# Optimization experiments

Measured on AMD Instinct MI355X. Metric: run time of the kernel, lower is better.

## Reference

```python
import jax, jax.numpy as jnp
import numpy as np

N = 131072          # total sampled proposals (flattened over batch)
D = 1024            # num_extractor_out
C = 21              # num_classes (VOC: 20 + background)


def setup_inputs() -> dict:
    key = jax.random.key(0)
    k1, k2, k3 = jax.random.split(key, 3)
    features = jax.random.normal(k1, (N, D), dtype=jnp.float32)
    # Linear weights stored as [in, out] so y = x @ W + b
    W_cls = jax.random.normal(k2, (D, C), dtype=jnp.float32) * (1.0 / np.sqrt(D))
    b_cls = jnp.zeros((C,), dtype=jnp.float32)
    W_tf = jax.random.normal(k3, (D, C * 4), dtype=jnp.float32) * (1.0 / np.sqrt(D))
    b_tf = jnp.zeros((C * 4,), dtype=jnp.float32)
    return {"features": features, "W_cls": W_cls, "b_cls": b_cls, "W_tf": W_tf, "b_tf": b_tf}


def reference(features, W_cls, b_cls, W_tf, b_tf):
    # ROI.forward with identity extractor / no pre/post transforms.
    proposal_classes = features @ W_cls + b_cls                    # [N, C]
    proposal_transformers = features @ W_tf + b_tf                 # [N, C*4]
    proposal_transformers = proposal_transformers.reshape(features.shape[0], C, 4)
    return proposal_classes, proposal_transformers
```

## Files before the change

kernel.cpp:

```cpp
#include <hip/hip_runtime.h>
#include <hip/hip_bf16.h>

#define NROWS 131072
#define DK    1024
#define CCLS  21
#define CTF   84
#define NCOL  105
#define NKT   (DK/32)
#define NCT   7
#define BM    128

typedef __attribute__((ext_vector_type(4))) float f32x4;
typedef __attribute__((ext_vector_type(8))) short bf16x8;

__device__ __forceinline__ unsigned short f2bf_rne(float x) {
    union { float f; unsigned u; } v; v.f = x;
    unsigned r = v.u + 0x7fffu + ((v.u >> 16) & 1u);
    return (unsigned short)(r >> 16);
}

__device__ __forceinline__ unsigned pack2(float lo, float hi) {
    union { float f; unsigned u; } a, b; a.f = lo; b.f = hi;
    return ((a.u + 0x8000u) >> 16) | ((b.u + 0x8000u) & 0xffff0000u);
}

__device__ __forceinline__ bf16x8 cvt8(const f32x4 lo, const f32x4 hi) {
    union { unsigned u[4]; bf16x8 v; } r;
    r.u[0] = pack2(lo[0], lo[1]);
    r.u[1] = pack2(lo[2], lo[3]);
    r.u[2] = pack2(hi[0], hi[1]);
    r.u[3] = pack2(hi[2], hi[3]);
    return r.v;
}

__global__ void pack_B_kernel(const float* __restrict__ Wc,
                              const float* __restrict__ Wt,
                              unsigned short* __restrict__ Bp) {
    const int frag = blockIdx.x;
    const int kt = frag / NCT, ct = frag % NCT;
    const int lane = threadIdx.x;
    const int col = ct * 16 + (lane & 15);
    const int k0  = kt * 32 + ((lane >> 4) << 3);
    bf16x8 o;
#pragma unroll
    for (int j = 0; j < 8; ++j) {
        const int k = k0 + j;
        float v = 0.0f;
        if (col < CCLS)      v = Wc[k * CCLS + col];
        else if (col < NCOL) v = Wt[k * CTF + (col - CCLS)];
        o[j] = (short)f2bf_rne(v);
    }
    *reinterpret_cast<bf16x8*>(Bp + ((size_t)frag * 64 + lane) * 8) = o;
}

__global__ __launch_bounds__(256, 4)
void roi_gemm_kernel(const float* __restrict__ F,
                     const unsigned short* __restrict__ Bp,
                     const float* __restrict__ bcls,
                     const float* __restrict__ btf,
                     float* __restrict__ out) {
    const int t    = threadIdx.x;
    const int wave = t >> 6;
    const int lane = t & 63;
    const int fr   = lane & 15;
    const int fk   = (lane >> 4) * 8;

    const long rw = (long)blockIdx.x * BM + wave * 32;
    const float* pa0 = F + (size_t)(rw + fr) * DK + fk;
    const float* pa1 = pa0 + (size_t)16 * DK;

    f32x4 acc[2][NCT];
#pragma unroll
    for (int a = 0; a < 2; ++a)
#pragma unroll
        for (int b = 0; b < NCT; ++b)
            acc[a][b] = (f32x4){0.f, 0.f, 0.f, 0.f};

    const unsigned short* bb = Bp + (size_t)lane * 8;

    for (int kt = 0; kt < NKT; ++kt) {
        const f32x4 a0lo = *reinterpret_cast<const f32x4*>(pa0 + kt * 32);
        const f32x4 a0hi = *reinterpret_cast<const f32x4*>(pa0 + kt * 32 + 4);
        const f32x4 a1lo = *reinterpret_cast<const f32x4*>(pa1 + kt * 32);
        const f32x4 a1hi = *reinterpret_cast<const f32x4*>(pa1 + kt * 32 + 4);

        bf16x8 bfrag[NCT];
#pragma unroll
        for (int ct = 0; ct < NCT; ++ct)
            bfrag[ct] = *reinterpret_cast<const bf16x8*>(
                bb + ((size_t)kt * NCT + ct) * 64 * 8);

        const bf16x8 af0 = cvt8(a0lo, a0hi);
        const bf16x8 af1 = cvt8(a1lo, a1hi);

#pragma unroll
        for (int ct = 0; ct < NCT; ++ct) {
            acc[0][ct] = __builtin_amdgcn_mfma_f32_16x16x32_bf16(
                af0, bfrag[ct], acc[0][ct], 0, 0, 0);
            acc[1][ct] = __builtin_amdgcn_mfma_f32_16x16x32_bf16(
                af1, bfrag[ct], acc[1][ct], 0, 0, 0);
        }
    }

    float* out_tf = out + (size_t)NROWS * CCLS;
#pragma unroll
    for (int rt = 0; rt < 2; ++rt) {
        const long rbase = rw + rt * 16 + ((lane >> 4) << 2);
#pragma unroll
        for (int ct = 0; ct < NCT; ++ct) {
            const int col = ct * 16 + fr;
            if (col >= NCOL) continue;
            const float bias = (col < CCLS) ? bcls[col] : btf[col - CCLS];
#pragma unroll
            for (int j = 0; j < 4; ++j) {
                const long row = rbase + j;
                const float v = acc[rt][ct][j] + bias;
                if (col < CCLS) out[row * CCLS + col] = v;
                else            out_tf[row * CTF + (col - CCLS)] = v;
            }
        }
    }
}

extern "C" void kernel_launch(void* const* d_in, const int* in_sizes, int n_in,
                              void* d_out, int out_size, void* d_ws, size_t ws_size,
                              hipStream_t stream) {
    const float* F  = (const float*)d_in[0];
    const float* Wc = (const float*)d_in[1];
    const float* bc = (const float*)d_in[2];
    const float* Wt = (const float*)d_in[3];
    const float* bt = (const float*)d_in[4];
    unsigned short* Bp = (unsigned short*)d_ws;

    pack_B_kernel<<<NKT * NCT, 64, 0, stream>>>(Wc, Wt, Bp);
    roi_gemm_kernel<<<NROWS / BM, 256, 0, stream>>>(F, Bp, bc, bt, (float*)d_out);
}
```

Before: 172.1 us.

## Software-pipeline A loads four k-steps ahead with 16-row waves and 512-thread blocks

Each wave now handles 16 rows instead of 32, so a 128-row block uses 8 waves (512 threads). The k loop is unrolled by 4 with a rotating set of register stages, so fp32 feature loads are issued four k-tiles ahead of their conversion and MFMA use. The goal is to hide global-memory latency on this bandwidth-bound GEMM. In exchange, B fragments are loaded twice as often per row, since each wave covers half as many rows, and register pressure rises from the prefetch buffers.

```diff
diff --git a/kernel.cpp b/kernel.cpp
--- a/kernel.cpp
+++ b/kernel.cpp
@@ -24,12 +24,14 @@
     return ((a.u + 0x8000u) >> 16) | ((b.u + 0x8000u) & 0xffff0000u);
 }
 
-__device__ __forceinline__ bf16x8 cvt8(const f32x4 lo, const f32x4 hi) {
+struct Astage { f32x4 lo, hi; };
+
+__device__ __forceinline__ bf16x8 cvt8(const Astage& s) {
     union { unsigned u[4]; bf16x8 v; } r;
-    r.u[0] = pack2(lo[0], lo[1]);
-    r.u[1] = pack2(lo[2], lo[3]);
-    r.u[2] = pack2(hi[0], hi[1]);
-    r.u[3] = pack2(hi[2], hi[3]);
+    r.u[0] = pack2(s.lo[0], s.lo[1]);
+    r.u[1] = pack2(s.lo[2], s.lo[3]);
+    r.u[2] = pack2(s.hi[0], s.hi[1]);
+    r.u[3] = pack2(s.hi[2], s.hi[3]);
     return r.v;
 }
 
@@ -53,7 +55,7 @@
     *reinterpret_cast<bf16x8*>(Bp + ((size_t)frag * 64 + lane) * 8) = o;
 }
 
-__global__ __launch_bounds__(256, 4)
+__global__ __launch_bounds__(512, 4)
 void roi_gemm_kernel(const float* __restrict__ F,
                      const unsigned short* __restrict__ Bp,
                      const float* __restrict__ bcls,
@@ -65,59 +67,60 @@
     const int fr   = lane & 15;
     const int fk   = (lane >> 4) * 8;
 
-    const long rw = (long)blockIdx.x * BM + wave * 32;
-    const float* pa0 = F + (size_t)(rw + fr) * DK + fk;
-    const float* pa1 = pa0 + (size_t)16 * DK;
+    const long rw = (long)blockIdx.x * BM + wave * 16;
+    const float* pa = F + (size_t)(rw + fr) * DK + fk;
 
-    f32x4 acc[2][NCT];
+    f32x4 acc[NCT];
 #pragma unroll
-    for (int a = 0; a < 2; ++a)
-#pragma unroll
-        for (int b = 0; b < NCT; ++b)
-            acc[a][b] = (f32x4){0.f, 0.f, 0.f, 0.f};
+    for (int b = 0; b < NCT; ++b) acc[b] = (f32x4){0.f, 0.f, 0.f, 0.f};
 
     const unsigned short* bb = Bp + (size_t)lane * 8;
 
-    for (int kt = 0; kt < NKT; ++kt) {
-        const f32x4 a0lo = *reinterpret_cast<const f32x4*>(pa0 + kt * 32);
-        const f32x4 a0hi = *reinterpret_cast<const f32x4*>(pa0 + kt * 32 + 4);
-        const f32x4 a1lo = *reinterpret_cast<const f32x4*>(pa1 + kt * 32);
-        const f32x4 a1hi = *reinterpret_cast<const f32x4*>(pa1 + kt * 32 + 4);
+#define LOADA(S, KT) do { \
+    (S).lo = *reinterpret_cast<const f32x4*>(pa + (KT) * 32); \
+    (S).hi = *reinterpret_cast<const f32x4*>(pa + (KT) * 32 + 4); \
+} while (0)
 
-        bf16x8 bfrag[NCT];
-#pragma unroll
-        for (int ct = 0; ct < NCT; ++ct)
-            bfrag[ct] = *reinterpret_cast<const bf16x8*>(
-                bb + ((size_t)kt * NCT + ct) * 64 * 8);
+    Astage A0, A1, A2, A3;
+    LOADA(A0, 0); LOADA(A1, 1); LOADA(A2, 2); LOADA(A3, 3);
 
-        const bf16x8 af0 = cvt8(a0lo, a0hi);
-        const bf16x8 af1 = cvt8(a1lo, a1hi);
+#define STEP(S, KT) do { \
+    bf16x8 bfrag[NCT]; \
+    _Pragma("unroll") \
+    for (int ct = 0; ct < NCT; ++ct) \
+        bfrag[ct] = *reinterpret_cast<const bf16x8*>( \
+            bb + ((size_t)(KT) * NCT + ct) * 512); \
+    const bf16x8 af = cvt8(S); \
+    if ((KT) + 4 < NKT) LOADA(S, (KT) + 4); \
+    _Pragma("unroll") \
+    for (int ct = 0; ct < NCT; ++ct) \
+        acc[ct] = __builtin_amdgcn_mfma_f32_16x16x32_bf16( \
+            af, bfrag[ct], acc[ct], 0, 0, 0); \
+} while (0)
 
 #pragma unroll
-        for (int ct = 0; ct < NCT; ++ct) {
-            acc[0][ct] = __builtin_amdgcn_mfma_f32_16x16x32_bf16(
-                af0, bfrag[ct], acc[0][ct], 0, 0, 0);
-            acc[1][ct] = __builtin_amdgcn_mfma_f32_16x16x32_bf16(
-                af1, bfrag[ct], acc[1][ct], 0, 0, 0);
-        }
+    for (int kt = 0; kt < NKT; kt += 4) {
+        STEP(A0, kt + 0);
+        STEP(A1, kt + 1);
+        STEP(A2, kt + 2);
+        STEP(A3, kt + 3);
     }
+#undef STEP
+#undef LOADA
 
     float* out_tf = out + (size_t)NROWS * CCLS;
+    const long rbase = rw + ((lane >> 4) << 2);
 #pragma unroll
-    for (int rt = 0; rt < 2; ++rt) {
-        const long rbase = rw + rt * 16 + ((lane >> 4) << 2);
+    for (int ct = 0; ct < NCT; ++ct) {
+        const int col = ct * 16 + fr;
+        if (col >= NCOL) continue;
+        const float bias = (col < CCLS) ? bcls[col] : btf[col - CCLS];
 #pragma unroll
-        for (int ct = 0; ct < NCT; ++ct) {
-            const int col = ct * 16 + fr;
-            if (col >= NCOL) continue;
-            const float bias = (col < CCLS) ? bcls[col] : btf[col - CCLS];
-#pragma unroll
-            for (int j = 0; j < 4; ++j) {
-                const long row = rbase + j;
-                const float v = acc[rt][ct][j] + bias;
-                if (col < CCLS) out[row * CCLS + col] = v;
-                else            out_tf[row * CTF + (col - CCLS)] = v;
-            }
+        for (int j = 0; j < 4; ++j) {
+            const long row = rbase + j;
+            const float v = acc[ct][j] + bias;
+            if (col < CCLS) out[row * CCLS + col] = v;
+            else            out_tf[row * CTF + (col - CCLS)] = v;
         }
     }
 }
@@ -133,5 +136,5 @@
     unsigned short* Bp = (unsigned short*)d_ws;
 
     pack_B_kernel<<<NKT * NCT, 64, 0, stream>>>(Wc, Wt, Bp);
-    roi_gemm_kernel<<<NROWS / BM, 256, 0, stream>>>(F, Bp, bc, bt, (float*)d_out);
+    roi_gemm_kernel<<<NROWS / BM, 512, 0, stream>>>(F, Bp, bc, bt, (float*)d_out);
 }
```

Result: slower. 196.2 us (+14.0%).

## Stage feature tiles through LDS with async double-buffered global_load_lds

Applied to the files above, without the earlier changes.

Replaces per-lane direct global loads of the fp32 feature rows with asynchronous global-to-LDS loads into a double-buffered, XOR-swizzled shared tile of 64-wide K slabs. The next slab is prefetched while the current one is converted to bf16 and fed to MFMA, with manual vmcnt waits and scheduling barriers. The goal is to hide memory latency on this bandwidth-bound GEMM and make global reads fully coalesced. In exchange it uses 64KB of LDS per block and lowers the launch-bounds occupancy target from 4 to 2, so fewer waves are resident to cover latency.

```diff
diff --git a/kernel.cpp b/kernel.cpp
--- a/kernel.cpp
+++ b/kernel.cpp
@@ -6,12 +6,16 @@
 #define CCLS  21
 #define CTF   84
 #define NCOL  105
-#define NKT   (DK/32)
 #define NCT   7
 #define BM    128
+#define BKF   64
+#define NSLAB (DK / BKF)
 
 typedef __attribute__((ext_vector_type(4))) float f32x4;
 typedef __attribute__((ext_vector_type(8))) short bf16x8;
+
+typedef const __attribute__((address_space(1))) void GV;
+typedef __attribute__((address_space(3))) void LV;
 
 __device__ __forceinline__ unsigned short f2bf_rne(float x) {
     union { float f; unsigned u; } v; v.f = x;
@@ -24,7 +28,7 @@
     return ((a.u + 0x8000u) >> 16) | ((b.u + 0x8000u) & 0xffff0000u);
 }
 
-__device__ __forceinline__ bf16x8 cvt8(const f32x4 lo, const f32x4 hi) {
+__device__ __forceinline__ bf16x8 cvt8v(const f32x4 lo, const f32x4 hi) {
     union { unsigned u[4]; bf16x8 v; } r;
     r.u[0] = pack2(lo[0], lo[1]);
     r.u[1] = pack2(lo[2], lo[3]);
@@ -53,21 +57,26 @@
     *reinterpret_cast<bf16x8*>(Bp + ((size_t)frag * 64 + lane) * 8) = o;
 }
 
-__global__ __launch_bounds__(256, 4)
+__global__ __launch_bounds__(256, 2)
 void roi_gemm_kernel(const float* __restrict__ F,
                      const unsigned short* __restrict__ Bp,
                      const float* __restrict__ bcls,
                      const float* __restrict__ btf,
                      float* __restrict__ out) {
+    __shared__ float Alds[2][4][32][BKF];
+
     const int t    = threadIdx.x;
     const int wave = t >> 6;
     const int lane = t & 63;
     const int fr   = lane & 15;
-    const int fk   = (lane >> 4) * 8;
+    const int fq   = lane >> 4;
+    const int sw   = fr & 7;
 
     const long rw = (long)blockIdx.x * BM + wave * 32;
-    const float* pa0 = F + (size_t)(rw + fr) * DK + fk;
-    const float* pa1 = pa0 + (size_t)16 * DK;
+
+    const float* srcE = F + (size_t)(rw + fq) * DK + ((fr ^ fq) << 2);
+    const float* srcO = F + (size_t)(rw + fq) * DK + ((fr ^ (fq + 4)) << 2);
+    const unsigned short* bb = Bp + (size_t)lane * 8;
 
     f32x4 acc[2][NCT];
 #pragma unroll
@@ -76,36 +85,69 @@
         for (int b = 0; b < NCT; ++b)
             acc[a][b] = (f32x4){0.f, 0.f, 0.f, 0.f};
 
-    const unsigned short* bb = Bp + (size_t)lane * 8;
+#define STAGE(BUF, S) do {                                                   \
+    const float* _e = srcE + (size_t)(S) * BKF;                              \
+    const float* _o = srcO + (size_t)(S) * BKF;                              \
+    _Pragma("unroll")                                                        \
+    for (int q = 0; q < 8; ++q) {                                            \
+        const float* g = ((q & 1) ? _o : _e) + (size_t)q * 4 * DK;           \
+        __builtin_amdgcn_global_load_lds((GV*)g,                             \
+            (LV*)&Alds[BUF][wave][q * 4][0], 16, 0, 0);                      \
+    }                                                                        \
+} while (0)
 
-    for (int kt = 0; kt < NKT; ++kt) {
-        const f32x4 a0lo = *reinterpret_cast<const f32x4*>(pa0 + kt * 32);
-        const f32x4 a0hi = *reinterpret_cast<const f32x4*>(pa0 + kt * 32 + 4);
-        const f32x4 a1lo = *reinterpret_cast<const f32x4*>(pa1 + kt * 32);
-        const f32x4 a1hi = *reinterpret_cast<const f32x4*>(pa1 + kt * 32 + 4);
+    STAGE(0, 0);
 
-        bf16x8 bfrag[NCT];
+    for (int s = 0; s < NSLAB; ++s) {
+        const int buf = s & 1;
+
+        __builtin_amdgcn_sched_barrier(0);
+        bf16x8 bf[2][NCT];
 #pragma unroll
-        for (int ct = 0; ct < NCT; ++ct)
-            bfrag[ct] = *reinterpret_cast<const bf16x8*>(
-                bb + ((size_t)kt * NCT + ct) * 64 * 8);
+        for (int kt = 0; kt < 2; ++kt)
+#pragma unroll
+            for (int ct = 0; ct < NCT; ++ct)
+                bf[kt][ct] = *reinterpret_cast<const bf16x8*>(
+                    bb + ((size_t)((s * 2 + kt) * NCT + ct) * 512));
+        __builtin_amdgcn_sched_barrier(0);
 
-        const bf16x8 af0 = cvt8(a0lo, a0hi);
-        const bf16x8 af1 = cvt8(a1lo, a1hi);
+        if (s + 1 < NSLAB) {
+            STAGE((s + 1) & 1, s + 1);
+            __builtin_amdgcn_sched_barrier(0);
+            asm volatile("s_waitcnt vmcnt(8)" ::: "memory");
+        } else {
+            asm volatile("s_waitcnt vmcnt(0)" ::: "memory");
+        }
+        __builtin_amdgcn_sched_barrier(0);
 
 #pragma unroll
-        for (int ct = 0; ct < NCT; ++ct) {
-            acc[0][ct] = __builtin_amdgcn_mfma_f32_16x16x32_bf16(
-                af0, bfrag[ct], acc[0][ct], 0, 0, 0);
-            acc[1][ct] = __builtin_amdgcn_mfma_f32_16x16x32_bf16(
-                af1, bfrag[ct], acc[1][ct], 0, 0, 0);
+        for (int kt = 0; kt < 2; ++kt) {
+            bf16x8 af[2];
+#pragma unroll
+            for (int rt = 0; rt < 2; ++rt) {
+                const float* lpr = &Alds[buf][wave][rt * 16 + fr][0];
+                const int c0 = kt * 8 + fq * 2;
+                const f32x4 lo = *reinterpret_cast<const f32x4*>(
+                    lpr + (((c0 + 0) ^ sw) << 2));
+                const f32x4 hi = *reinterpret_cast<const f32x4*>(
+                    lpr + (((c0 + 1) ^ sw) << 2));
+                af[rt] = cvt8v(lo, hi);
+            }
+#pragma unroll
+            for (int ct = 0; ct < NCT; ++ct) {
+                acc[0][ct] = __builtin_amdgcn_mfma_f32_16x16x32_bf16(
+                    af[0], bf[kt][ct], acc[0][ct], 0, 0, 0);
+                acc[1][ct] = __builtin_amdgcn_mfma_f32_16x16x32_bf16(
+                    af[1], bf[kt][ct], acc[1][ct], 0, 0, 0);
+            }
         }
     }
+#undef STAGE
 
     float* out_tf = out + (size_t)NROWS * CCLS;
 #pragma unroll
     for (int rt = 0; rt < 2; ++rt) {
-        const long rbase = rw + rt * 16 + ((lane >> 4) << 2);
+        const long rbase = rw + rt * 16 + (fq << 2);
 #pragma unroll
         for (int ct = 0; ct < NCT; ++ct) {
             const int col = ct * 16 + fr;
@@ -132,6 +174,6 @@
     const float* bt = (const float*)d_in[4];
     unsigned short* Bp = (unsigned short*)d_ws;
 
-    pack_B_kernel<<<NKT * NCT, 64, 0, stream>>>(Wc, Wt, Bp);
+    pack_B_kernel<<<NCT * (DK / 32), 64, 0, stream>>>(Wc, Wt, Bp);
     roi_gemm_kernel<<<NROWS / BM, 256, 0, stream>>>(F, Bp, bc, bt, (float*)d_out);
 }
```

Result: faster. 153.3 us (-10.9%).

## Split K across waves with LDS-staged bf16 A tile and cross-wave reduction

Applied to the files above, without the earlier changes.

Each block now handles 32 rows instead of 128, and its four waves each take a quarter of the K dimension rather than separate row groups. Each block first stages its A rows into 64KB of LDS as bf16 using coalesced float4 loads and an XOR swizzle. Waves then run MFMA over their K slice with double-buffered B fragment loads, and partial sums are reduced through LDS before the biased results are written. This targets poor coalescing of A loads and latency exposure, at the cost of 64KB LDS per block (lower occupancy, launch bounds 2) and extra reduction traffic.

```diff
diff --git a/kernel.cpp b/kernel.cpp
--- a/kernel.cpp
+++ b/kernel.cpp
@@ -6,12 +6,12 @@
 #define CCLS  21
 #define CTF   84
 #define NCOL  105
-#define NKT   (DK/32)
 #define NCT   7
-#define BM    128
+#define BM    32
 
 typedef __attribute__((ext_vector_type(4))) float f32x4;
 typedef __attribute__((ext_vector_type(8))) short bf16x8;
+typedef __attribute__((ext_vector_type(2))) unsigned int u32x2;
 
 __device__ __forceinline__ unsigned short f2bf_rne(float x) {
     union { float f; unsigned u; } v; v.f = x;
@@ -22,15 +22,6 @@
 __device__ __forceinline__ unsigned pack2(float lo, float hi) {
     union { float f; unsigned u; } a, b; a.f = lo; b.f = hi;
     return ((a.u + 0x8000u) >> 16) | ((b.u + 0x8000u) & 0xffff0000u);
-}
-
-__device__ __forceinline__ bf16x8 cvt8(const f32x4 lo, const f32x4 hi) {
-    union { unsigned u[4]; bf16x8 v; } r;
-    r.u[0] = pack2(lo[0], lo[1]);
-    r.u[1] = pack2(lo[2], lo[3]);
-    r.u[2] = pack2(hi[0], hi[1]);
-    r.u[3] = pack2(hi[2], hi[3]);
-    return r.v;
 }
 
 __global__ void pack_B_kernel(const float* __restrict__ Wc,
@@ -53,21 +44,50 @@
     *reinterpret_cast<bf16x8*>(Bp + ((size_t)frag * 64 + lane) * 8) = o;
 }
 
-__global__ __launch_bounds__(256, 4)
+__global__ __launch_bounds__(256, 2)
 void roi_gemm_kernel(const float* __restrict__ F,
                      const unsigned short* __restrict__ Bp,
                      const float* __restrict__ bcls,
                      const float* __restrict__ btf,
                      float* __restrict__ out) {
+    __shared__ __align__(16) unsigned char smem[65536];
+
     const int t    = threadIdx.x;
     const int wave = t >> 6;
     const int lane = t & 63;
     const int fr   = lane & 15;
-    const int fk   = (lane >> 4) * 8;
+    const int fq   = lane >> 4;
+    const long rw  = (long)blockIdx.x * BM;
 
-    const long rw = (long)blockIdx.x * BM + wave * 32;
-    const float* pa0 = F + (size_t)(rw + fr) * DK + fk;
-    const float* pa1 = pa0 + (size_t)16 * DK;
+    {
+        const int r0 = wave * 8;
+#pragma unroll
+        for (int p = 0; p < 4; ++p) {
+            f32x4 v[2][4];
+#pragma unroll
+            for (int e = 0; e < 2; ++e) {
+                const int R = r0 + p * 2 + e;
+                const float* src = F + (size_t)(rw + R) * DK + lane * 4;
+#pragma unroll
+                for (int q = 0; q < 4; ++q)
+                    v[e][q] = *reinterpret_cast<const f32x4*>(src + q * 256);
+            }
+#pragma unroll
+            for (int e = 0; e < 2; ++e) {
+                const int R = r0 + p * 2 + e;
+#pragma unroll
+                for (int q = 0; q < 4; ++q) {
+                    u32x2 d;
+                    d[0] = pack2(v[e][q][0], v[e][q][1]);
+                    d[1] = pack2(v[e][q][2], v[e][q][3]);
+                    const int ch = (q * 32 + (lane >> 1)) ^ (R & 7);
+                    *reinterpret_cast<u32x2*>(
+                        smem + R * 2048 + ch * 16 + (lane & 1) * 8) = d;
+                }
+            }
+        }
+    }
+    __syncthreads();
 
     f32x4 acc[2][NCT];
 #pragma unroll
@@ -77,48 +97,67 @@
             acc[a][b] = (f32x4){0.f, 0.f, 0.f, 0.f};
 
     const unsigned short* bb = Bp + (size_t)lane * 8;
+    const int w8 = wave * 8;
 
-    for (int kt = 0; kt < NKT; ++kt) {
-        const f32x4 a0lo = *reinterpret_cast<const f32x4*>(pa0 + kt * 32);
-        const f32x4 a0hi = *reinterpret_cast<const f32x4*>(pa0 + kt * 32 + 4);
-        const f32x4 a1lo = *reinterpret_cast<const f32x4*>(pa1 + kt * 32);
-        const f32x4 a1hi = *reinterpret_cast<const f32x4*>(pa1 + kt * 32 + 4);
+    bf16x8 bfr[2][NCT];
+#pragma unroll
+    for (int ct = 0; ct < NCT; ++ct)
+        bfr[0][ct] = *reinterpret_cast<const bf16x8*>(
+            bb + ((size_t)(w8 * NCT + ct) * 512));
 
-        bf16x8 bfrag[NCT];
 #pragma unroll
-        for (int ct = 0; ct < NCT; ++ct)
-            bfrag[ct] = *reinterpret_cast<const bf16x8*>(
-                bb + ((size_t)kt * NCT + ct) * 64 * 8);
-
-        const bf16x8 af0 = cvt8(a0lo, a0hi);
-        const bf16x8 af1 = cvt8(a1lo, a1hi);
-
+    for (int j = 0; j < 8; ++j) {
+        const int cur = j & 1;
+        if (j + 1 < 8) {
+#pragma unroll
+            for (int ct = 0; ct < NCT; ++ct)
+                bfr[cur ^ 1][ct] = *reinterpret_cast<const bf16x8*>(
+                    bb + ((size_t)((w8 + j + 1) * NCT + ct) * 512));
+        }
+        const int ktg = w8 + j;
+        bf16x8 a[2];
+#pragma unroll
+        for (int rt = 0; rt < 2; ++rt) {
+            const int R = rt * 16 + fr;
+            const int ch = (ktg * 4 + fq) ^ (R & 7);
+            a[rt] = *reinterpret_cast<const bf16x8*>(smem + R * 2048 + ch * 16);
+        }
 #pragma unroll
         for (int ct = 0; ct < NCT; ++ct) {
             acc[0][ct] = __builtin_amdgcn_mfma_f32_16x16x32_bf16(
-                af0, bfrag[ct], acc[0][ct], 0, 0, 0);
+                a[0], bfr[cur][ct], acc[0][ct], 0, 0, 0);
             acc[1][ct] = __builtin_amdgcn_mfma_f32_16x16x32_bf16(
-                af1, bfrag[ct], acc[1][ct], 0, 0, 0);
+                a[1], bfr[cur][ct], acc[1][ct], 0, 0, 0);
         }
     }
 
+    __syncthreads();
+#pragma unroll
+    for (int rt = 0; rt < 2; ++rt)
+#pragma unroll
+        for (int ct = 0; ct < NCT; ++ct)
+            *reinterpret_cast<f32x4*>(
+                smem + (size_t)(wave * 14 + rt * 7 + ct) * 1024 + lane * 16) =
+                acc[rt][ct];
+    __syncthreads();
+
+    const float* sf = reinterpret_cast<const float*>(smem);
     float* out_tf = out + (size_t)NROWS * CCLS;
+    const int rl = t >> 2;
+    const int rj = t & 3;
 #pragma unroll
-    for (int rt = 0; rt < 2; ++rt) {
-        const long rbase = rw + rt * 16 + ((lane >> 4) << 2);
-#pragma unroll
-        for (int ct = 0; ct < NCT; ++ct) {
-            const int col = ct * 16 + fr;
-            if (col >= NCOL) continue;
-            const float bias = (col < CCLS) ? bcls[col] : btf[col - CCLS];
-#pragma unroll
-            for (int j = 0; j < 4; ++j) {
-                const long row = rbase + j;
-                const float v = acc[rt][ct][j] + bias;
-                if (col < CCLS) out[row * CCLS + col] = v;
-                else            out_tf[row * CTF + (col - CCLS)] = v;
-            }
-        }
+    for (int s = 0; s < 14; ++s) {
+        const int rt = s / 7, ct = s % 7;
+        const int col = ct * 16 + (rl & 15);
+        if (col >= NCOL) continue;
+        const float v = sf[0 * 3584 + s * 256 + t] +
+                        sf[1 * 3584 + s * 256 + t] +
+                        sf[2 * 3584 + s * 256 + t] +
+                        sf[3 * 3584 + s * 256 + t] +
+                        ((col < CCLS) ? bcls[col] : btf[col - CCLS]);
+        const long row = rw + rt * 16 + ((rl >> 4) << 2) + rj;
+        if (col < CCLS) out[row * CCLS + col] = v;
+        else            out_tf[row * CTF + (col - CCLS)] = v;
     }
 }
 
@@ -132,6 +171,7 @@
     const float* bt = (const float*)d_in[4];
     unsigned short* Bp = (unsigned short*)d_ws;
 
-    pack_B_kernel<<<NKT * NCT, 64, 0, stream>>>(Wc, Wt, Bp);
-    roi_gemm_kernel<<<NROWS / BM, 256, 0, stream>>>(F, Bp, bc, bt, (float*)d_out);
+    pack_B_kernel<<<NCT * (DK / 32), 64, 0, stream>>>(Wc, Wt, Bp);
+    roi_gemm_kernel<<<NROWS / BM, 256, 0, stream>>>(F, Bp, bc, bt,
+                                                    (float*)d_out);
 }
```

Result: faster. 163.1 us (-5.2%).
